# Kernel optimization log

Hardware: AMD Instinct MI355X
Metric: run time of the kernel (lower is better)

The kernel has to match this reference:

```python
import jax, jax.numpy as jnp
import numpy as np

K = 3            # num_neighbors
C_IN = 128       # in_channels (== out_channels, required by fusion_kernel)
C_OUT = 128
B, H, W = 2, 64, 512
EPS = 1e-5       # BatchNorm eps (eval mode, running stats)


def _unfold(x, k):
    # F.unfold(x, k, padding=k//2).view(B, C, k*k, H*W); patch index = kh*k + kw
    b, c, h, w = x.shape
    p = k // 2
    xp = jnp.pad(x, ((0, 0), (0, 0), (p, p), (p, p)))
    patches = jnp.stack(
        [xp[:, :, i:i + h, j:j + w] for i in range(k) for j in range(k)], axis=2
    )  # (B, C, k*k, H, W)
    return patches.reshape(b, c, k * k, h * w)


def _conv1x1(x, w):
    # 1x1 Conv2d (bias=False) on (B, C, K^2, HW)
    return jnp.einsum('oc,bcnp->bonp', w, x)


def _bn(x, g, b, m, v):
    # BatchNorm2d in eval mode with running stats
    scale = (g / jnp.sqrt(v + EPS))[None, :, None, None]
    shift = (b - m * g / jnp.sqrt(v + EPS))[None, :, None, None]
    return x * scale + shift


def setup_inputs() -> dict:
    key = jax.random.key(0)
    ks = jax.random.split(key, 9)
    f32 = jnp.float32
    features = jax.random.normal(ks[0], (B, C_IN, H, W), f32)
    cart = jax.random.normal(ks[1], (B, 3, H, W), f32)
    mask = jax.random.bernoulli(ks[2], 0.9, (B, 1, H, W))

    def bn_params(k, c):
        k1, k2, k3, k4 = jax.random.split(k, 4)
        g = 1.0 + 0.1 * jax.random.normal(k1, (c,), f32)
        b = 0.1 * jax.random.normal(k2, (c,), f32)
        m = 0.1 * jax.random.normal(k3, (c,), f32)
        v = jax.random.uniform(k4, (c,), f32, 0.5, 1.5)
        return g, b, m, v

    pw = jax.random.normal(ks[3], (C_OUT, 3), f32) / jnp.sqrt(3.0)
    pg, pb, pm, pv = bn_params(ks[4], C_OUT)
    fw = jax.random.normal(ks[5], (C_OUT, C_IN), f32) / jnp.sqrt(float(C_IN))
    fg, fb, fm, fv = bn_params(ks[6], C_OUT)
    ew = jax.random.normal(ks[7], (3, C_OUT), f32) / jnp.sqrt(float(C_OUT))
    eg, eb, em, ev = bn_params(ks[8], 3)
    return dict(features=features, cart=cart, mask=mask,
                pw=pw, pg=pg, pb=pb, pm=pm, pv=pv,
                fw=fw, fg=fg, fb=fb, fm=fm, fv=fv,
                ew=ew, eg=eg, eb=eb, em=em, ev=ev)


def reference(features, cart, mask, pw, pg, pb, pm, pv,
              fw, fg, fb, fm, fv, ew, eg, eb, em, ev):
    b, c, h, w = features.shape
    fdt = features.dtype
    fe = _unfold(features, K)                      # (B, C, K^2, HW)
    cc = _unfold(cart, K)                          # (B, 3, K^2, HW)
    mu = _unfold(mask.astype(fdt), K)              # (B, 1, K^2, HW)
    center = (K * K) // 2
    rel = cc - cc[:, :, center:center + 1]         # relative coordinates
    pos = jax.nn.relu(_bn(_conv1x1(rel, pw), pg, pb, pm, pv))
    fe = jax.nn.relu(_bn(_conv1x1(fe, fw), fg, fb, fm, fv)) + pos
    geo = jnp.max(fe * mu, axis=2, keepdims=True)  # max_pool over K^2 neighbors
    e2c = _bn(_conv1x1(geo, ew), eg, eb, em, ev).reshape(b, 3, h, w)
    cart_out = cart + e2c * mask.astype(cart.dtype)
    return geo.reshape(b, -1, h, w), cart_out
```

## Files before the change

### kernel.cpp

```cpp
#include <hip/hip_runtime.h>

typedef unsigned short u16;
typedef unsigned int u32;
typedef unsigned char u8;

#define HW 32768
#define NPX 65536
#define GEO_SIZE 8388608
#define EPS 1e-5f

#define OFF_PWP   0
#define OFF_EWP   512
#define OFF_SHE   1024
#define OFF_FLG   1028
#define OFF_SHF   1088
#define W2T_OFF   8192
#define EAP_OFF   131072
#define T_OFF     8388608

#define LDS_STRIDE 136

typedef __bf16 bf16x8 __attribute__((ext_vector_type(8)));
typedef float f32x4 __attribute__((ext_vector_type(4)));
typedef float f32x2 __attribute__((ext_vector_type(2)));

__device__ __forceinline__ float bf2f(u16 u){ return __uint_as_float(((u32)u) << 16); }
__device__ __forceinline__ u16 f2bf(float f){
  u32 x = __float_as_uint(f);
  return (u16)((x + 0x7fffu + ((x >> 16) & 1u)) >> 16);
}
__device__ __forceinline__ float bflo(u32 w){ return __uint_as_float(w << 16); }
__device__ __forceinline__ float bfhi(u32 w){ return __uint_as_float(w & 0xffff0000u); }

__device__ __forceinline__ f32x2 pk_fma(f32x2 a, f32x2 b, f32x2 c){
  return __builtin_elementwise_fma(a, b, c);
}
__device__ __forceinline__ f32x2 pk_max(f32x2 a, f32x2 b){
  return __builtin_elementwise_max(a, b);
}

__device__ __forceinline__ float ldp(const void* p, int i, bool isbf){
  return isbf ? bf2f(((const u16*)p)[i]) : ((const float*)p)[i];
}

__device__ __forceinline__ bool sniff_bf16(const void* fv){
  const u16* w = (const u16*)fv;
  int hits = 0;
  for (int i = 0; i < 32; i++) {
    float v = bf2f(w[i]);
    hits += (v >= 0.45f && v <= 1.55f) ? 1 : 0;
  }
  return hits >= 26;
}

__device__ __forceinline__ int sniff_mask(const void* mask){
  const u8* mb = (const u8*)mask;
  int c01 = 0, ones = 0;
  for (int i = 0; i < 64; i++) { u8 v = mb[i]; c01 += (v <= 1); ones += (v == 1); }
  if (c01 == 64) return (ones >= 24) ? 0 : 1;
  const u16* mw = (const u16*)mask;
  int c3f = 0;
  for (int i = 0; i < 32; i++) c3f += (mw[i] == 0x3F80);
  return (c3f >= 22) ? 2 : 3;
}

__device__ __forceinline__ float mask_at(const void* m, int gi, int enc){
  if (enc == 0) return ((const u8*)m)[gi]  ? 1.f : 0.f;
  if (enc == 1) return ((const int*)m)[gi] ? 1.f : 0.f;
  if (enc == 2) return ((const u16*)m)[gi] ? 1.f : 0.f;
  return (((const float*)m)[gi] != 0.f) ? 1.f : 0.f;
}

__global__ __launch_bounds__(256) void prep_kernel(
    const void* __restrict__ pw, const void* __restrict__ pg,
    const void* __restrict__ pb, const void* __restrict__ pm,
    const void* __restrict__ pv,
    const void* __restrict__ fw, const void* __restrict__ fg,
    const void* __restrict__ fb, const void* __restrict__ fm,
    const void* __restrict__ fv,
    const void* __restrict__ ew, const void* __restrict__ eg,
    const void* __restrict__ eb, const void* __restrict__ em,
    const void* __restrict__ ev,
    const void* __restrict__ mask,
    float* __restrict__ ws){
  int blk = blockIdx.x, tid = threadIdx.x;
  bool isbf = sniff_bf16(fv);
  if (blk < 32) {
    int p = blk * 256 + tid;
    int o = p >> 6;
    float sf = ldp(fg, o, isbf) * __frsqrt_rn(ldp(fv, o, isbf) + EPS);
    u32 outv;
    if (isbf) {
      u32 in = ((const u32*)fw)[p];
      outv = (u32)f2bf(sf * bf2f((u16)(in & 0xffff))) |
             ((u32)f2bf(sf * bf2f((u16)(in >> 16))) << 16);
    } else {
      const float* fwp = (const float*)fw;
      outv = (u32)f2bf(sf * fwp[2 * p]) | ((u32)f2bf(sf * fwp[2 * p + 1]) << 16);
    }
    ((u32*)((char*)ws + W2T_OFF))[p] = outv;
    return;
  }
  int o = tid;
  if (o == 0) {
    ws[OFF_FLG]     = isbf ? 1.f : 0.f;
    ws[OFF_FLG + 1] = (float)sniff_mask(mask);
  }
  if (o < 128) {
    float sf = ldp(fg, o, isbf) * __frsqrt_rn(ldp(fv, o, isbf) + EPS);
    ws[OFF_SHF + o] = ldp(fb, o, isbf) - ldp(fm, o, isbf) * sf;
    float sp = ldp(pg, o, isbf) * __frsqrt_rn(ldp(pv, o, isbf) + EPS);
    float4* pwp = (float4*)(ws + OFF_PWP);
    pwp[o] = make_float4(sp * ldp(pw, o * 3 + 0, isbf),
                         sp * ldp(pw, o * 3 + 1, isbf),
                         sp * ldp(pw, o * 3 + 2, isbf),
                         ldp(pb, o, isbf) - ldp(pm, o, isbf) * sp);
    float se0 = ldp(eg, 0, isbf) * __frsqrt_rn(ldp(ev, 0, isbf) + EPS);
    float se1 = ldp(eg, 1, isbf) * __frsqrt_rn(ldp(ev, 1, isbf) + EPS);
    float se2 = ldp(eg, 2, isbf) * __frsqrt_rn(ldp(ev, 2, isbf) + EPS);
    float4* ewp = (float4*)(ws + OFF_EWP);
    ewp[o] = make_float4(se0 * ldp(ew, 0 * 128 + o, isbf),
                         se1 * ldp(ew, 1 * 128 + o, isbf),
                         se2 * ldp(ew, 2 * 128 + o, isbf), 0.f);
    if (o < 3) {
      float se = ldp(eg, o, isbf) * __frsqrt_rn(ldp(ev, o, isbf) + EPS);
      ws[OFF_SHE + o] = ldp(eb, o, isbf) - ldp(em, o, isbf) * se;
    }
  }
}

__global__ __launch_bounds__(256) void stage1_kernel(const void* __restrict__ feat,
                                                     const float* __restrict__ ws,
                                                     u16* __restrict__ t){
  __shared__ u16 lds[128 * LDS_STRIDE];
  int tid = threadIdx.x;
  bool isbf = ws[OFF_FLG] > 0.5f;
  int pxg = blockIdx.x * 128;
  int b = pxg >> 15, hw0 = pxg & 32767;

  {
    int cp = tid & 63, q = tid >> 6;
    int c0 = cp * 2;
    long e0 = (long)(b * 128 + c0) * HW + hw0 + q * 32;
    u16* base = lds + (q * 32) * LDS_STRIDE + c0;
    if (isbf) {
      const uint4* g0 = (const uint4*)((const u16*)feat + e0);
      const uint4* g1 = (const uint4*)((const u16*)feat + e0 + HW);
#pragma unroll
      for (int i = 0; i < 4; i++) {
        uint4 a = g0[i], c = g1[i];
        u32 av[4] = {a.x, a.y, a.z, a.w};
        u32 cv[4] = {c.x, c.y, c.z, c.w};
#pragma unroll
        for (int k = 0; k < 4; k++) {
          u32 lo = (av[k] & 0xffffu) | (cv[k] << 16);
          u32 hi = (av[k] >> 16) | (cv[k] & 0xffff0000u);
          *(u32*)(base + (i * 8 + k * 2 + 0) * LDS_STRIDE) = lo;
          *(u32*)(base + (i * 8 + k * 2 + 1) * LDS_STRIDE) = hi;
        }
      }
    } else {
      const float4* g0 = (const float4*)((const float*)feat + e0);
      const float4* g1 = (const float4*)((const float*)feat + e0 + HW);
#pragma unroll
      for (int i = 0; i < 8; i++) {
        float4 a = g0[i], c = g1[i];
        float av[4] = {a.x, a.y, a.z, a.w};
        float cv[4] = {c.x, c.y, c.z, c.w};
#pragma unroll
        for (int k = 0; k < 4; k++) {
          u32 v = (u32)f2bf(av[k]) | ((u32)f2bf(cv[k]) << 16);
          *(u32*)(base + (i * 4 + k) * LDS_STRIDE) = v;
        }
      }
    }
  }
  __syncthreads();

  int wave = tid >> 6, lane = tid & 63;
  int ln = lane & 15, quad = lane >> 4;
  int pxw = wave * 32;
  const uint4* W = (const uint4*)((const char*)ws + W2T_OFF);

  f32x4 acc[8][2];
#pragma unroll
  for (int ot = 0; ot < 8; ot++)
#pragma unroll
    for (int pt = 0; pt < 2; pt++) acc[ot][pt] = (f32x4){0.f, 0.f, 0.f, 0.f};

#pragma unroll
  for (int ks = 0; ks < 4; ks++) {
    bf16x8 a[8], bfr[2];
#pragma unroll
    for (int ot = 0; ot < 8; ot++)
      a[ot] = __builtin_bit_cast(bf16x8, W[(ot * 16 + ln) * 16 + ks * 4 + quad]);
#pragma unroll
    for (int pt = 0; pt < 2; pt++)
      bfr[pt] = __builtin_bit_cast(bf16x8,
          *(const uint4*)(lds + (pxw + pt * 16 + ln) * LDS_STRIDE + ks * 32 + quad * 8));
#pragma unroll
    for (int ot = 0; ot < 8; ot++)
#pragma unroll
      for (int pt = 0; pt < 2; pt++)
        acc[ot][pt] = __builtin_amdgcn_mfma_f32_16x16x32_bf16(a[ot], bfr[pt], acc[ot][pt], 0, 0, 0);
  }
  __syncthreads();

  const float* shf = ws + OFF_SHF;
#pragma unroll
  for (int ot = 0; ot < 8; ot++) {
#pragma unroll
    for (int r = 0; r < 4; r++) {
      int o = ot * 16 + quad * 4 + r;
      float s = shf[o];
#pragma unroll
      for (int pt = 0; pt < 2; pt++) {
        float v = fmaxf(acc[ot][pt][r] + s, 0.f);
        lds[o * LDS_STRIDE + pxw + pt * 16 + ln] = f2bf(v);
      }
    }
  }
  __syncthreads();
  {
    int o = tid >> 1, half = tid & 1;
    const u16* src = lds + o * LDS_STRIDE + half * 64;
    uint4* dst = (uint4*)(t + o * NPX + pxg + half * 64);
#pragma unroll
    for (int k = 0; k < 8; k++) dst[k] = *(const uint4*)(src + k * 8);
  }
}

__global__ __launch_bounds__(256) void stage2_kernel(const void* __restrict__ cart,
                                                     const float* __restrict__ ws,
                                                     const void* __restrict__ rawmask,
                                                     const u16* __restrict__ t,
                                                     float* __restrict__ eap,
                                                     void* __restrict__ out){
  int tid = threadIdx.x;
  int pxb = blockIdx.x & 127, grp = blockIdx.x >> 7;
  int px0 = pxb * 512 + tid * 2;
  int b = px0 >> 15, hw = px0 & 32767;
  int h = hw >> 9, w = hw & 511;
  bool isbf = ws[OFF_FLG] > 0.5f;
  int enc = (int)ws[OFF_FLG + 1];

  f32x2 rel2[9][3];
  f32x2 mv2[9];
  {
    float cr[12][3];
    float mm[12];
#pragma unroll
    for (int r = 0; r < 3; r++) {
#pragma unroll
      for (int c = 0; c < 4; c++) {
        int idx = r * 4 + c;
        int h2 = h + r - 1, w2 = w + c - 1;
        bool ok = ((unsigned)h2 < 64u) && ((unsigned)w2 < 512u);
        int hw2 = ok ? ((h2 << 9) | w2) : hw;
        int gi = b * HW + hw2;
        mm[idx] = ok ? mask_at(rawmask, gi, enc) : 0.f;
#pragma unroll
        for (int d = 0; d < 3; d++)
          cr[idx][d] = isbf ? bf2f(((const u16*)cart)[(b * 3 + d) * HW + hw2])
                            : ((const float*)cart)[(b * 3 + d) * HW + hw2];
      }
    }
#pragma unroll
    for (int r = 0; r < 3; r++)
#pragma unroll
      for (int cc = 0; cc < 3; cc++) {
        int n = r * 3 + cc;
        mv2[n] = (f32x2){mm[r * 4 + cc], mm[r * 4 + cc + 1]};
#pragma unroll
        for (int d = 0; d < 3; d++)
          rel2[n][d] = (f32x2){cr[r * 4 + cc][d] - cr[5][d],
                               cr[r * 4 + cc + 1][d] - cr[6][d]};
      }
  }

  const float4* pwp = (const float4*)(ws + OFF_PWP);
  const float4* ewp = (const float4*)(ws + OFF_EWP);
  f32x2 eA = {0.f, 0.f}, eB = {0.f, 0.f}, eC = {0.f, 0.f};
  u16* o16 = (u16*)out;
  float* of = (float*)out;
  const f32x2 zero2 = {0.f, 0.f};

#pragma unroll 4
  for (int j = 0; j < 32; j++) {
    int o = grp * 32 + j;
    const u16* tb = t + o * NPX + b * HW;
    u32 tw[3][3];
#pragma unroll
    for (int r = 0; r < 3; r++) {
      const u32* rp = (const u32*)(tb + (h + r - 1) * 512 + (w - 2));
      tw[r][0] = rp[0]; tw[r][1] = rp[1]; tw[r][2] = rp[2];
    }
    float4 P = pwp[o];
    f32x2 Px = {P.x, P.x}, Py = {P.y, P.y}, Pz = {P.z, P.z}, Pw = {P.w, P.w};
    f32x2 g = {0.f, 0.f};
#pragma unroll
    for (int r = 0; r < 3; r++) {
      float tm1 = bfhi(tw[r][0]);
      float t0  = bflo(tw[r][1]);
      float tp1 = bfhi(tw[r][1]);
      float tp2 = bflo(tw[r][2]);
      f32x2 tv[3] = {{tm1, t0}, {t0, tp1}, {tp1, tp2}};
#pragma unroll
      for (int cc = 0; cc < 3; cc++) {
        int n = r * 3 + cc;
        f32x2 pos = pk_max(pk_fma(Px, rel2[n][0],
                           pk_fma(Py, rel2[n][1],
                           pk_fma(Pz, rel2[n][2], Pw))), zero2);
        g = pk_max(g, (tv[cc] + pos) * mv2[n]);
      }
    }
    int gi = (b * 128 + o) * HW + hw;
    if (isbf) *(u32*)(o16 + gi) = (u32)f2bf(g.x) | ((u32)f2bf(g.y) << 16);
    else { of[gi] = g.x; of[gi + 1] = g.y; }
    float4 E = ewp[o];
    eA = pk_fma((f32x2){E.x, E.x}, g, eA);
    eB = pk_fma((f32x2){E.y, E.y}, g, eB);
    eC = pk_fma((f32x2){E.z, E.z}, g, eC);
  }
  *(f32x2*)(eap + (grp * 3 + 0) * NPX + px0) = eA;
  *(f32x2*)(eap + (grp * 3 + 1) * NPX + px0) = eB;
  *(f32x2*)(eap + (grp * 3 + 2) * NPX + px0) = eC;
}

__global__ __launch_bounds__(256) void final_kernel(const void* __restrict__ cart,
                                                    const float* __restrict__ ws,
                                                    const void* __restrict__ rawmask,
                                                    const float* __restrict__ eap,
                                                    void* __restrict__ out){
  int px0 = (blockIdx.x * 256 + threadIdx.x) * 2;
  int b = px0 >> 15, hw = px0 & 32767;
  bool isbf = ws[OFF_FLG] > 0.5f;
  int enc = (int)ws[OFF_FLG + 1];
  f32x2 s0 = {0.f, 0.f}, s1 = {0.f, 0.f}, s2 = {0.f, 0.f};
#pragma unroll
  for (int g = 0; g < 4; g++) {
    s0 += *(const f32x2*)(eap + (g * 3 + 0) * NPX + px0);
    s1 += *(const f32x2*)(eap + (g * 3 + 1) * NPX + px0);
    s2 += *(const f32x2*)(eap + (g * 3 + 2) * NPX + px0);
  }
  float m0 = mask_at(rawmask, b * HW + hw, enc);
  float m1 = mask_at(rawmask, b * HW + hw + 1, enc);
  float she0 = ws[OFF_SHE], she1 = ws[OFF_SHE + 1], she2 = ws[OFF_SHE + 2];
  float c0a, c0b, c1a, c1b, c2a, c2b;
  if (isbf) {
    const u16* cb = (const u16*)cart + b * 3 * HW;
    c0a = bf2f(cb[hw]); c0b = bf2f(cb[hw + 1]);
    c1a = bf2f(cb[HW + hw]); c1b = bf2f(cb[HW + hw + 1]);
    c2a = bf2f(cb[2 * HW + hw]); c2b = bf2f(cb[2 * HW + hw + 1]);
  } else {
    const float* cb = (const float*)cart + b * 3 * HW;
    c0a = cb[hw]; c0b = cb[hw + 1];
    c1a = cb[HW + hw]; c1b = cb[HW + hw + 1];
    c2a = cb[2 * HW + hw]; c2b = cb[2 * HW + hw + 1];
  }
  float r0a = c0a + (s0.x + she0) * m0, r0b = c0b + (s0.y + she0) * m1;
  float r1a = c1a + (s1.x + she1) * m0, r1b = c1b + (s1.y + she1) * m1;
  float r2a = c2a + (s2.x + she2) * m0, r2b = c2b + (s2.y + she2) * m1;
  int cbase = GEO_SIZE + b * 3 * HW + hw;
  if (isbf) {
    u16* o16 = (u16*)out;
    *(u32*)(o16 + cbase)          = (u32)f2bf(r0a) | ((u32)f2bf(r0b) << 16);
    *(u32*)(o16 + cbase + HW)     = (u32)f2bf(r1a) | ((u32)f2bf(r1b) << 16);
    *(u32*)(o16 + cbase + 2 * HW) = (u32)f2bf(r2a) | ((u32)f2bf(r2b) << 16);
  } else {
    float* of = (float*)out;
    of[cbase] = r0a; of[cbase + 1] = r0b;
    of[cbase + HW] = r1a; of[cbase + HW + 1] = r1b;
    of[cbase + 2 * HW] = r2a; of[cbase + 2 * HW + 1] = r2b;
  }
}

extern "C" void kernel_launch(void* const* d_in, const int* in_sizes, int n_in,
                              void* d_out, int out_size, void* d_ws, size_t ws_size,
                              hipStream_t stream) {
  const void* feat = d_in[0];
  const void* cart = d_in[1];
  const void* mask = d_in[2];
  float* ws  = (float*)d_ws;
  float* eap = (float*)((char*)d_ws + EAP_OFF);
  u16*  t    = (u16*)((char*)d_ws + T_OFF);

  hipLaunchKernelGGL(prep_kernel, dim3(33), dim3(256), 0, stream,
                     d_in[3], d_in[4], d_in[5], d_in[6], d_in[7],
                     d_in[8], d_in[9], d_in[10], d_in[11], d_in[12],
                     d_in[13], d_in[14], d_in[15], d_in[16], d_in[17],
                     mask, ws);
  hipLaunchKernelGGL(stage1_kernel, dim3(512), dim3(256), 0, stream, feat, ws, t);
  hipLaunchKernelGGL(stage2_kernel, dim3(512), dim3(256), 0, stream, cart, ws, mask, t, eap, d_out);
  hipLaunchKernelGGL(final_kernel, dim3(128), dim3(256), 0, stream, cart, ws, mask, eap, d_out);
}
```

Baseline: 166.0 us.

## Halve stage1 tile, use XOR-swizzled LDS layout, and split stage2 channels finer

Stage1 now handles 64 pixels per block instead of 128, doubling the grid. It loads features with per-thread scalar strided reads and stores them into an XOR-swizzled 256-byte-row LDS layout to avoid bank conflicts, with one MFMA pixel tile per wave. Stage2 splits the output channels into 8 groups of 16 instead of 4 of 32 for more blocks, and the final kernel sums 8 partials. The goal is more parallelism and fewer LDS conflicts, at the cost of less coalesced global loads, reloading weights per block, and extra partial-sum traffic.

```diff
diff --git a/kernel.cpp b/kernel.cpp
--- a/kernel.cpp
+++ b/kernel.cpp
@@ -17,8 +17,6 @@
 #define W2T_OFF   8192
 #define EAP_OFF   131072
 #define T_OFF     8388608
-
-#define LDS_STRIDE 136
 
 typedef __bf16 bf16x8 __attribute__((ext_vector_type(8)));
 typedef float f32x4 __attribute__((ext_vector_type(4)));
@@ -132,77 +130,69 @@
 __global__ __launch_bounds__(256) void stage1_kernel(const void* __restrict__ feat,
                                                      const float* __restrict__ ws,
                                                      u16* __restrict__ t){
-  __shared__ u16 lds[128 * LDS_STRIDE];
+  __shared__ u16 lds[128 * 72];
   int tid = threadIdx.x;
   bool isbf = ws[OFF_FLG] > 0.5f;
-  int pxg = blockIdx.x * 128;
+  int pxg = blockIdx.x * 64;
   int b = pxg >> 15, hw0 = pxg & 32767;
 
   {
-    int cp = tid & 63, q = tid >> 6;
-    int c0 = cp * 2;
-    long e0 = (long)(b * 128 + c0) * HW + hw0 + q * 32;
-    u16* base = lds + (q * 32) * LDS_STRIDE + c0;
+    int l = tid & 63, cg = tid >> 6;
+    int ch0 = cg * 32;
+    int base = (b * 128 + ch0) * HW + hw0 + l;
+    char* rowp = (char*)lds + l * 256;
+    int xs = l & 15;
     if (isbf) {
-      const uint4* g0 = (const uint4*)((const u16*)feat + e0);
-      const uint4* g1 = (const uint4*)((const u16*)feat + e0 + HW);
-#pragma unroll
-      for (int i = 0; i < 4; i++) {
-        uint4 a = g0[i], c = g1[i];
-        u32 av[4] = {a.x, a.y, a.z, a.w};
-        u32 cv[4] = {c.x, c.y, c.z, c.w};
-#pragma unroll
-        for (int k = 0; k < 4; k++) {
-          u32 lo = (av[k] & 0xffffu) | (cv[k] << 16);
-          u32 hi = (av[k] >> 16) | (cv[k] & 0xffff0000u);
-          *(u32*)(base + (i * 8 + k * 2 + 0) * LDS_STRIDE) = lo;
-          *(u32*)(base + (i * 8 + k * 2 + 1) * LDS_STRIDE) = hi;
-        }
+      const u16* fp = (const u16*)feat;
+      u16 v[32];
+#pragma unroll
+      for (int i = 0; i < 32; i++) v[i] = fp[base + i * HW];
+#pragma unroll
+      for (int g = 0; g < 4; g++) {
+        uint4 pk;
+        pk.x = (u32)v[g*8+0] | ((u32)v[g*8+1] << 16);
+        pk.y = (u32)v[g*8+2] | ((u32)v[g*8+3] << 16);
+        pk.z = (u32)v[g*8+4] | ((u32)v[g*8+5] << 16);
+        pk.w = (u32)v[g*8+6] | ((u32)v[g*8+7] << 16);
+        *(uint4*)(rowp + ((((cg << 2) | g) ^ xs) << 4)) = pk;
       }
     } else {
-      const float4* g0 = (const float4*)((const float*)feat + e0);
-      const float4* g1 = (const float4*)((const float*)feat + e0 + HW);
-#pragma unroll
-      for (int i = 0; i < 8; i++) {
-        float4 a = g0[i], c = g1[i];
-        float av[4] = {a.x, a.y, a.z, a.w};
-        float cv[4] = {c.x, c.y, c.z, c.w};
-#pragma unroll
-        for (int k = 0; k < 4; k++) {
-          u32 v = (u32)f2bf(av[k]) | ((u32)f2bf(cv[k]) << 16);
-          *(u32*)(base + (i * 4 + k) * LDS_STRIDE) = v;
-        }
+      const float* fp = (const float*)feat;
+      float v[32];
+#pragma unroll
+      for (int i = 0; i < 32; i++) v[i] = fp[base + i * HW];
+#pragma unroll
+      for (int g = 0; g < 4; g++) {
+        uint4 pk;
+        pk.x = (u32)f2bf(v[g*8+0]) | ((u32)f2bf(v[g*8+1]) << 16);
+        pk.y = (u32)f2bf(v[g*8+2]) | ((u32)f2bf(v[g*8+3]) << 16);
+        pk.z = (u32)f2bf(v[g*8+4]) | ((u32)f2bf(v[g*8+5]) << 16);
+        pk.w = (u32)f2bf(v[g*8+6]) | ((u32)f2bf(v[g*8+7]) << 16);
+        *(uint4*)(rowp + ((((cg << 2) | g) ^ xs) << 4)) = pk;
       }
     }
   }
   __syncthreads();
 
-  int wave = tid >> 6, lane = tid & 63;
+  int wv = tid >> 6, lane = tid & 63;
   int ln = lane & 15, quad = lane >> 4;
-  int pxw = wave * 32;
   const uint4* W = (const uint4*)((const char*)ws + W2T_OFF);
-
-  f32x4 acc[8][2];
-#pragma unroll
-  for (int ot = 0; ot < 8; ot++)
-#pragma unroll
-    for (int pt = 0; pt < 2; pt++) acc[ot][pt] = (f32x4){0.f, 0.f, 0.f, 0.f};
-
+  f32x4 acc[8];
+#pragma unroll
+  for (int ot = 0; ot < 8; ot++) acc[ot] = (f32x4){0.f, 0.f, 0.f, 0.f};
+
+  const char* rbase = (const char*)lds + (wv * 16 + ln) * 256;
 #pragma unroll
   for (int ks = 0; ks < 4; ks++) {
-    bf16x8 a[8], bfr[2];
+    bf16x8 bb = __builtin_bit_cast(bf16x8,
+        *(const uint4*)(rbase + ((((ks << 2) | quad) ^ ln) << 4)));
+    bf16x8 a[8];
 #pragma unroll
     for (int ot = 0; ot < 8; ot++)
       a[ot] = __builtin_bit_cast(bf16x8, W[(ot * 16 + ln) * 16 + ks * 4 + quad]);
 #pragma unroll
-    for (int pt = 0; pt < 2; pt++)
-      bfr[pt] = __builtin_bit_cast(bf16x8,
-          *(const uint4*)(lds + (pxw + pt * 16 + ln) * LDS_STRIDE + ks * 32 + quad * 8));
-#pragma unroll
     for (int ot = 0; ot < 8; ot++)
-#pragma unroll
-      for (int pt = 0; pt < 2; pt++)
-        acc[ot][pt] = __builtin_amdgcn_mfma_f32_16x16x32_bf16(a[ot], bfr[pt], acc[ot][pt], 0, 0, 0);
+      acc[ot] = __builtin_amdgcn_mfma_f32_16x16x32_bf16(a[ot], bb, acc[ot], 0, 0, 0);
   }
   __syncthreads();
 
@@ -212,21 +202,17 @@
 #pragma unroll
     for (int r = 0; r < 4; r++) {
       int o = ot * 16 + quad * 4 + r;
-      float s = shf[o];
-#pragma unroll
-      for (int pt = 0; pt < 2; pt++) {
-        float v = fmaxf(acc[ot][pt][r] + s, 0.f);
-        lds[o * LDS_STRIDE + pxw + pt * 16 + ln] = f2bf(v);
-      }
+      float v = fmaxf(acc[ot][r] + shf[o], 0.f);
+      lds[o * 72 + wv * 16 + ln] = f2bf(v);
     }
   }
   __syncthreads();
   {
     int o = tid >> 1, half = tid & 1;
-    const u16* src = lds + o * LDS_STRIDE + half * 64;
-    uint4* dst = (uint4*)(t + o * NPX + pxg + half * 64);
-#pragma unroll
-    for (int k = 0; k < 8; k++) dst[k] = *(const uint4*)(src + k * 8);
+    const u16* src = lds + o * 72 + half * 32;
+    uint4* dst = (uint4*)(t + o * NPX + pxg + half * 32);
+#pragma unroll
+    for (int k = 0; k < 4; k++) dst[k] = *(const uint4*)(src + k * 8);
   }
 }
 
@@ -286,8 +272,8 @@
   const f32x2 zero2 = {0.f, 0.f};
 
 #pragma unroll 4
-  for (int j = 0; j < 32; j++) {
-    int o = grp * 32 + j;
+  for (int j = 0; j < 16; j++) {
+    int o = grp * 16 + j;
     const u16* tb = t + o * NPX + b * HW;
     u32 tw[3][3];
 #pragma unroll
@@ -338,7 +324,7 @@
   int enc = (int)ws[OFF_FLG + 1];
   f32x2 s0 = {0.f, 0.f}, s1 = {0.f, 0.f}, s2 = {0.f, 0.f};
 #pragma unroll
-  for (int g = 0; g < 4; g++) {
+  for (int g = 0; g < 8; g++) {
     s0 += *(const f32x2*)(eap + (g * 3 + 0) * NPX + px0);
     s1 += *(const f32x2*)(eap + (g * 3 + 1) * NPX + px0);
     s2 += *(const f32x2*)(eap + (g * 3 + 2) * NPX + px0);
@@ -390,7 +376,7 @@
                      d_in[8], d_in[9], d_in[10], d_in[11], d_in[12],
                      d_in[13], d_in[14], d_in[15], d_in[16], d_in[17],
                      mask, ws);
-  hipLaunchKernelGGL(stage1_kernel, dim3(512), dim3(256), 0, stream, feat, ws, t);
-  hipLaunchKernelGGL(stage2_kernel, dim3(512), dim3(256), 0, stream, cart, ws, mask, t, eap, d_out);
+  hipLaunchKernelGGL(stage1_kernel, dim3(1024), dim3(256), 0, stream, feat, ws, t);
+  hipLaunchKernelGGL(stage2_kernel, dim3(1024), dim3(256), 0, stream, cart, ws, mask, t, eap, d_out);
   hipLaunchKernelGGL(final_kernel, dim3(128), dim3(256), 0, stream, cart, ws, mask, eap, d_out);
 }
```

After: 166.0 us. No clear change (-0.0%).
